# Kernel optimization log

Measured on AMD Instinct MI355X. Metric: run time of the kernel, lower is better.

The kernel has to match this reference:

```python
import jax, jax.numpy as jnp
import numpy as np

B, S, E, W = 16, 1024, 1024, 7  # batch, seq_len, emb_dim, (odd) window size
PAD_VAL = 0.0  # padding_idx used as constant pad value in the torch code


def setup_inputs() -> dict:
    key = jax.random.key(0)
    kx, kw, kb = jax.random.split(key, 3)
    x = jax.random.normal(kx, (B, S, E), dtype=jnp.float32)
    # per-position Linear(E*W -> W): torch default init U(-1/sqrt(fan_in), 1/sqrt(fan_in))
    bound = 1.0 / np.sqrt(W * E)
    weight = jax.random.uniform(kw, (S, W, W * E), minval=-bound, maxval=bound, dtype=jnp.float32)
    bias = jax.random.uniform(kb, (S, W), minval=-bound, maxval=bound, dtype=jnp.float32)
    return {"x": x, "weight": weight, "bias": bias}


def reference(x, weight, bias):
    Bb, Ss, Ee = x.shape
    Wn = bias.shape[1]
    hw = Wn // 2
    # constant-pad the sequence dim with padding_idx value
    padded = jnp.pad(x, ((0, 0), (hw, hw), (0, 0)), constant_values=PAD_VAL)
    # gather all windows at once: windows[b, t, w, e] = padded[b, t + w, e]
    idx = jnp.arange(Ss)[:, None] + jnp.arange(Wn)[None, :]  # [S, W]
    windows = padded[:, idx, :]  # [B, S, W, E]
    # per-position linear on flattened window: weight[t] is [W_out=W, W*E]
    w4 = weight.reshape(Ss, Wn, Wn, Ee)  # [t, v, w, e]
    logits = jnp.einsum('btwe,tvwe->btv', windows, w4) + bias[None, :, :]  # [B, S, W]
    gates = jax.nn.sigmoid(logits)
    # gated sum over window, then tanh
    out = jnp.tanh(jnp.einsum('btw,btwe->bte', gates, windows))  # [B, S, E]
    return out
```

## Files before the change

kernel.cpp:

```cpp
#include <hip/hip_runtime.h>


#define Bq 16
#define Sq 1024
#define Eq 1024
#define Wq 7
#define HWq 3

__global__ __launch_bounds__(256, 4) void soft_reorder_kernel(
    const float* __restrict__ x,
    const float* __restrict__ weight,
    const float* __restrict__ bias,
    float* __restrict__ out)
{
    const int bid = blockIdx.x;
    const int t = (bid & 7) * (Sq / 8) + (bid >> 3);
    const int tid = threadIdx.x;
    const int b = tid >> 4;
    const int j = tid & 15;

    __shared__ float gates[Bq][Wq + 1];

    const float* wt = weight + (size_t)t * (Wq * Wq * Eq);

    float4 acc[Wq];
#pragma unroll
    for (int v = 0; v < Wq; ++v) acc[v] = make_float4(0.f, 0.f, 0.f, 0.f);

#pragma unroll
    for (int w = 0; w < Wq; ++w) {
        const int row = t + w - HWq;
        if ((unsigned)row < (unsigned)Sq) {
            const float* xr = x + ((size_t)b * Sq + row) * Eq;
            const float* wr = wt + w * Eq;
            for (int ee = j * 4; ee < Eq; ee += 64) {
                const float4 xv = *(const float4*)(xr + ee);
#pragma unroll
                for (int v = 0; v < Wq; ++v) {
                    const float4 wv = *(const float4*)(wr + (size_t)v * (Wq * Eq) + ee);
                    acc[v].x += xv.x * wv.x;
                    acc[v].y += xv.y * wv.y;
                    acc[v].z += xv.z * wv.z;
                    acc[v].w += xv.w * wv.w;
                }
            }
        }
    }

#pragma unroll
    for (int v = 0; v < Wq; ++v) {
        float s = acc[v].x + acc[v].y + acc[v].z + acc[v].w;
        s += __shfl_xor(s, 1, 16);
        s += __shfl_xor(s, 2, 16);
        s += __shfl_xor(s, 4, 16);
        s += __shfl_xor(s, 8, 16);
        if (j == 0) {
            const float logit = s + bias[t * Wq + v];
            gates[b][v] = 1.0f / (1.0f + __expf(-logit));
        }
    }
    __syncthreads();

    const int e = tid * 4;
    for (int bb = 0; bb < Bq; ++bb) {
        float g[Wq];
#pragma unroll
        for (int w = 0; w < Wq; ++w) g[w] = gates[bb][w];

        float4 a = make_float4(0.f, 0.f, 0.f, 0.f);
#pragma unroll
        for (int w = 0; w < Wq; ++w) {
            const int row = t + w - HWq;
            if ((unsigned)row < (unsigned)Sq) {
                const float4 xv = *(const float4*)(x + ((size_t)bb * Sq + row) * Eq + e);
                a.x += g[w] * xv.x;
                a.y += g[w] * xv.y;
                a.z += g[w] * xv.z;
                a.w += g[w] * xv.w;
            }
        }
        float4 o;
        o.x = 1.0f - 2.0f / (1.0f + __expf(2.0f * a.x));
        o.y = 1.0f - 2.0f / (1.0f + __expf(2.0f * a.y));
        o.z = 1.0f - 2.0f / (1.0f + __expf(2.0f * a.z));
        o.w = 1.0f - 2.0f / (1.0f + __expf(2.0f * a.w));
        *(float4*)(out + ((size_t)bb * Sq + t) * Eq + e) = o;
    }
}

extern "C" void kernel_launch(void* const* d_in, const int* in_sizes, int n_in,
                              void* d_out, int out_size, void* d_ws, size_t ws_size,
                              hipStream_t stream) {
    const float* x = (const float*)d_in[0];
    const float* weight = (const float*)d_in[1];
    const float* bias = (const float*)d_in[2];
    float* out = (float*)d_out;

    soft_reorder_kernel<<<Sq, 256, 0, stream>>>(x, weight, bias, out);
}
```

Before: 476.9 us.

## Register-block logits over four batches to reuse weight loads per thread

Restructures the logit phase so each thread holds one set of 7 weight float4s and applies it to 4 batch rows, instead of reloading weights for each batch row. Each thread now covers fixed E slices, with a wave-level shuffle followed by a shared-memory cross-wave reduction to form the gates. The aim is to cut redundant weight traffic through L1/L2 and raise arithmetic per load. In exchange it uses more registers (occupancy hint lowered from 4 to 2) and adds an extra barrier and reduction step.

```diff
diff --git a/kernel.cpp b/kernel.cpp
--- a/kernel.cpp
+++ b/kernel.cpp
@@ -6,8 +6,10 @@
 #define Eq 1024
 #define Wq 7
 #define HWq 3
+#define WEq (Wq * Eq)
+#define WWEq (Wq * WEq)
 
-__global__ __launch_bounds__(256, 4) void soft_reorder_kernel(
+__global__ __launch_bounds__(256, 2) void soft_reorder_kernel(
     const float* __restrict__ x,
     const float* __restrict__ weight,
     const float* __restrict__ bias,
@@ -16,52 +18,82 @@
     const int bid = blockIdx.x;
     const int t = (bid & 7) * (Sq / 8) + (bid >> 3);
     const int tid = threadIdx.x;
-    const int b = tid >> 4;
-    const int j = tid & 15;
+    const int bg = tid >> 6;
+    const int ks = tid & 63;
 
-    __shared__ float gates[Bq][Wq + 1];
+    __shared__ float red[4][4][28];
+    __shared__ float gates[Bq][8];
 
-    const float* wt = weight + (size_t)t * (Wq * Wq * Eq);
+    const float* wt = weight + (size_t)t * WWEq;
 
-    float4 acc[Wq];
+    float acc[4][7];
 #pragma unroll
-    for (int v = 0; v < Wq; ++v) acc[v] = make_float4(0.f, 0.f, 0.f, 0.f);
+    for (int bi = 0; bi < 4; ++bi)
+#pragma unroll
+        for (int v = 0; v < Wq; ++v) acc[bi][v] = 0.f;
 
 #pragma unroll
-    for (int w = 0; w < Wq; ++w) {
-        const int row = t + w - HWq;
-        if ((unsigned)row < (unsigned)Sq) {
-            const float* xr = x + ((size_t)b * Sq + row) * Eq;
-            const float* wr = wt + w * Eq;
-            for (int ee = j * 4; ee < Eq; ee += 64) {
-                const float4 xv = *(const float4*)(xr + ee);
+    for (int i4 = 0; i4 < 4; ++i4) {
+        const int e = (ks + i4 * 64) * 4;
 #pragma unroll
-                for (int v = 0; v < Wq; ++v) {
-                    const float4 wv = *(const float4*)(wr + (size_t)v * (Wq * Eq) + ee);
-                    acc[v].x += xv.x * wv.x;
-                    acc[v].y += xv.y * wv.y;
-                    acc[v].z += xv.z * wv.z;
-                    acc[v].w += xv.w * wv.w;
+        for (int w = 0; w < Wq; ++w) {
+            const int row = t + w - HWq;
+            if ((unsigned)row < (unsigned)Sq) {
+                float4 wv[Wq];
+#pragma unroll
+                for (int v = 0; v < Wq; ++v)
+                    wv[v] = *(const float4*)(wt + (size_t)v * WEq + w * Eq + e);
+#pragma unroll
+                for (int bi = 0; bi < 4; ++bi) {
+                    const int b = bg * 4 + bi;
+                    const float4 xv = *(const float4*)(x + ((size_t)b * Sq + row) * Eq + e);
+#pragma unroll
+                    for (int v = 0; v < Wq; ++v) {
+                        acc[bi][v] = fmaf(xv.x, wv[v].x, acc[bi][v]);
+                        acc[bi][v] = fmaf(xv.y, wv[v].y, acc[bi][v]);
+                        acc[bi][v] = fmaf(xv.z, wv[v].z, acc[bi][v]);
+                        acc[bi][v] = fmaf(xv.w, wv[v].w, acc[bi][v]);
+                    }
                 }
             }
         }
     }
 
 #pragma unroll
-    for (int v = 0; v < Wq; ++v) {
-        float s = acc[v].x + acc[v].y + acc[v].z + acc[v].w;
-        s += __shfl_xor(s, 1, 16);
-        s += __shfl_xor(s, 2, 16);
-        s += __shfl_xor(s, 4, 16);
-        s += __shfl_xor(s, 8, 16);
-        if (j == 0) {
-            const float logit = s + bias[t * Wq + v];
-            gates[b][v] = 1.0f / (1.0f + __expf(-logit));
+    for (int bi = 0; bi < 4; ++bi) {
+#pragma unroll
+        for (int v = 0; v < Wq; ++v) {
+            float s = acc[bi][v];
+            s += __shfl_xor(s, 1);
+            s += __shfl_xor(s, 2);
+            s += __shfl_xor(s, 4);
+            s += __shfl_xor(s, 8);
+            acc[bi][v] = s;
         }
+    }
+    if ((ks & 15) == 0) {
+        const int q = ks >> 4;
+#pragma unroll
+        for (int bi = 0; bi < 4; ++bi)
+#pragma unroll
+            for (int v = 0; v < Wq; ++v)
+                red[bg][q][bi * 7 + v] = acc[bi][v];
     }
     __syncthreads();
 
-    const int e = tid * 4;
+    if (tid < 4 * 28) {
+        const int g = tid / 28;
+        const int r = tid - g * 28;
+        const int bi = r / 7;
+        const int v = r - bi * 7;
+        const float s = red[g][0][r] + red[g][1][r] + red[g][2][r] + red[g][3][r];
+        const float logit = s + bias[t * Wq + v];
+        gates[g * 4 + bi][v] = 1.0f / (1.0f + __expf(-logit));
+    }
+    __syncthreads();
+
+    const int e2 = tid * 4;
+#pragma unroll 2
     for (int bb = 0; bb < Bq; ++bb) {
         float g[Wq];
 #pragma unroll
@@ -72,7 +104,7 @@
         for (int w = 0; w < Wq; ++w) {
             const int row = t + w - HWq;
             if ((unsigned)row < (unsigned)Sq) {
-                const float4 xv = *(const float4*)(x + ((size_t)bb * Sq + row) * Eq + e);
+                const float4 xv = *(const float4*)(x + ((size_t)bb * Sq + row) * Eq + e2);
                 a.x += g[w] * xv.x;
                 a.y += g[w] * xv.y;
                 a.z += g[w] * xv.z;
@@ -84,7 +116,7 @@
         o.y = 1.0f - 2.0f / (1.0f + __expf(2.0f * a.y));
         o.z = 1.0f - 2.0f / (1.0f + __expf(2.0f * a.z));
         o.w = 1.0f - 2.0f / (1.0f + __expf(2.0f * a.w));
-        *(float4*)(out + ((size_t)bb * Sq + t) * Eq + e) = o;
+        *(float4*)(out + ((size_t)bb * Sq + t) * Eq + e2) = o;
     }
 }
 
```

Result: faster. 394.8 us (-17.2%).
